# Optimization experiments

Measured on AMD Instinct MI355X. Metric: run time of the kernel, lower is better.

Reference implementation:

```python
import jax, jax.numpy as jnp
import numpy as np

ALPHA = 0.1        # dt / tau = 1 / 10
SIGMA_REC = 0.03
SIGMA_INP = 0.03


def setup_inputs() -> dict:
    key = jax.random.key(0)
    ks = jax.random.split(key, 7)
    n, N, num_inputs, num_outputs, T, B = 128, 1024, 6, 2, 512, 256
    u = jax.random.normal(ks[0], (num_inputs, T, B), dtype=jnp.float32)
    rec_noise = jax.random.normal(ks[1], (B, T, n), dtype=jnp.float32)
    inp_noise = jax.random.normal(ks[2], (B, T, num_inputs), dtype=jnp.float32)
    W_inp = jax.random.normal(ks[3], (n, num_inputs), dtype=jnp.float32) / np.float32(np.sqrt(num_inputs))
    # spectral-ish scaling keeps the leaky RNN stable over 512 steps
    W_rec = jax.random.normal(ks[4], (n, n), dtype=jnp.float32) * np.float32(0.9 / np.sqrt(n))
    W_out = jax.random.normal(ks[5], (num_outputs, n), dtype=jnp.float32) / np.float32(np.sqrt(n))
    # q is orthonormalized via SVD in the torch module (make_orthonormal)
    q0 = np.asarray(jax.random.uniform(ks[6], (n, N)), dtype=np.float32)
    U, _, Vh = np.linalg.svd(q0, full_matrices=False)
    q = jnp.asarray((U @ Vh).astype(np.float32))
    return dict(u=u, rec_noise=rec_noise, inp_noise=inp_noise,
                W_inp=W_inp, W_rec=W_rec, W_out=W_out, q=q)


def reference(u, rec_noise, inp_noise, W_inp, W_rec, W_out, q):
    # u: (num_inputs, T, B); noise tensors already batch-major (B, T, .)
    B = u.shape[-1]
    n = W_rec.shape[0]
    rn = jnp.sqrt(2.0 / ALPHA * SIGMA_REC ** 2) * rec_noise      # (B, T, n)
    inoise = jnp.sqrt(2.0 / ALPHA * SIGMA_INP ** 2) * inp_noise  # (B, T, num_inputs)
    ub = jnp.swapaxes(u, 0, -1)                                  # (B, T, num_inputs)
    x0 = jnp.zeros((B, n), dtype=u.dtype)                        # initial state self.x = 0

    def step(x, ins):
        u_t, in_t, rn_t = ins
        x_new = (1.0 - ALPHA) * x + ALPHA * (
            jax.nn.relu(x @ W_rec.T + (u_t + in_t) @ W_inp.T) + rn_t)
        return x_new, x_new

    # T-1 update steps using inputs at t = 0 .. T-2 (matches the torch loop)
    xs_in = (jnp.swapaxes(ub, 0, 1)[:-1],
             jnp.swapaxes(inoise, 0, 1)[:-1],
             jnp.swapaxes(rn, 0, 1)[:-1])
    _, xs = jax.lax.scan(step, x0, xs_in)                        # (T-1, B, n)
    states = jnp.concatenate([x0[:, None, :], jnp.swapaxes(xs, 0, 1)], axis=1)  # (B, T, n)

    outputs = jnp.swapaxes(states @ W_out.T, 0, -1)              # (num_outputs, T, B)
    states_embedded = jnp.swapaxes(states @ q, 0, -1)            # (N, T, B)
    return states_embedded, outputs
```

## Files before the change

### kernel.cpp

```cpp
#include <hip/hip_runtime.h>
#include <hip/hip_bf16.h>

#define T_STEPS 512
#define BATCH   256
#define NN      128
#define NEMB    1024
#define M_ROWS  (T_STEPS * BATCH)
#define NOISE_K 0.13416407864998738f
#define CH      8
#define NCHUNK  (T_STEPS / CH)

typedef short s16x8 __attribute__((ext_vector_type(8)));
typedef float f32x4 __attribute__((ext_vector_type(4)));

__device__ __forceinline__ unsigned short f2bf(float f) {
  union { float f; unsigned u; } v; v.f = f;
  unsigned r = v.u + 0x7fffu + ((v.u >> 16) & 1u);
  return (unsigned short)(r >> 16);
}
__device__ __forceinline__ float bf2f(unsigned short s) {
  union { unsigned u; float f; } v; v.u = ((unsigned)s) << 16;
  return v.f;
}
__device__ __forceinline__ float rdlane(float v, int l) {
  return __uint_as_float(__builtin_amdgcn_readlane(__float_as_uint(v), l));
}

__device__ __forceinline__ void light_barrier() {
  asm volatile("s_waitcnt lgkmcnt(0)" ::: "memory");
  __builtin_amdgcn_s_barrier();
  asm volatile("" ::: "memory");
}

__global__ __launch_bounds__(128, 1) void rnn_step_kernel(
    const float* __restrict__ u,
    const float* __restrict__ rec_noise,
    const float* __restrict__ inp_noise,
    const float* __restrict__ W_inp,
    const float* __restrict__ W_rec,
    unsigned short* __restrict__ states)
{
  const int b    = blockIdx.x;
  const int tid  = threadIdx.x;
  const int lane = tid & 63;

  __shared__ float xbuf[2][NN];
  __shared__ float rns[2][CH * NN];
  __shared__ float us[2][CH][8];

  const f32x4* wr = (const f32x4*)(W_rec + tid * NN);
  f32x4 w4[32];
  #pragma unroll
  for (int c = 0; c < 32; ++c) w4[c] = wr[c];

  float winp[6];
  #pragma unroll
  for (int j = 0; j < 6; ++j) winp[j] = W_inp[tid * 6 + j];

  const int ts6 = tid / 6, j6 = tid - ts6 * 6;

  xbuf[0][tid] = 0.f;
  states[b * NN + tid] = 0;

  {
    const f32x4* src = (const f32x4*)(rec_noise + (size_t)b * T_STEPS * NN);
    *(f32x4*)&rns[0][tid * 8]     = src[tid * 2];
    *(f32x4*)&rns[0][tid * 8 + 4] = src[tid * 2 + 1];
    if (tid < 48) {
      float uu = u[j6 * (T_STEPS * BATCH) + ts6 * BATCH + b];
      float in = inp_noise[((size_t)b * T_STEPS + ts6) * 6 + j6];
      us[0][ts6][j6] = uu + NOISE_K * in;
    }
  }
  __syncthreads();

  float xr = 0.f;
  for (int c = 0; c < NCHUNK; ++c) {
    const int cb = c & 1;

    f32x4 pf0 = {0.f, 0.f, 0.f, 0.f}, pf1 = {0.f, 0.f, 0.f, 0.f};
    float u_pf = 0.f, in_pf = 0.f;
    if (c < NCHUNK - 1) {
      const f32x4* src =
          (const f32x4*)(rec_noise + ((size_t)b * T_STEPS + (c + 1) * CH) * NN);
      pf0 = src[tid * 2];
      pf1 = src[tid * 2 + 1];
      if (tid < 48) {
        const int tt = (c + 1) * CH + ts6;
        u_pf  = u[j6 * (T_STEPS * BATCH) + tt * BATCH + b];
        in_pf = inp_noise[((size_t)b * T_STEPS + tt) * 6 + j6];
      }
    }

    #pragma unroll
    for (int ts = 0; ts < CH; ++ts) {
      const int t = c * CH + ts;
      if (t > T_STEPS - 2) break;
      const int cur = ts & 1, nxt = cur ^ 1;

      float2 vx = *(const float2*)&xbuf[cur][lane * 2];

      float a0 = 0.f, a1 = 0.f, a2 = 0.f, a3 = 0.f;
      #pragma unroll
      for (int kp = 0; kp < 64; ++kp) {
        const float x0 = rdlane(vx.x, kp);
        const float x1 = rdlane(vx.y, kp);
        const float we0 = w4[kp >> 1][(kp & 1) * 2];
        const float we1 = w4[kp >> 1][(kp & 1) * 2 + 1];
        if (kp & 1) { a2 = fmaf(we0, x0, a2); a3 = fmaf(we1, x1, a3); }
        else        { a0 = fmaf(we0, x0, a0); a1 = fmaf(we1, x1, a1); }
      }
      float acc = (a0 + a1) + (a2 + a3);

      float inp = 0.f;
      #pragma unroll
      for (int j = 0; j < 6; ++j) inp = fmaf(winp[j], us[cb][ts][j], inp);

      const float pre = acc + inp;
      const float r   = pre > 0.f ? pre : 0.f;
      const float xn  = 0.9f * xr + 0.1f * (r + NOISE_K * rns[cb][ts * NN + tid]);
      xr = xn;

      xbuf[nxt][tid] = xn;
      states[((t + 1) * BATCH + b) * NN + tid] = f2bf(xn);

      light_barrier();
    }

    if (c < NCHUNK - 1) {
      *(f32x4*)&rns[cb ^ 1][tid * 8]     = pf0;
      *(f32x4*)&rns[cb ^ 1][tid * 8 + 4] = pf1;
      if (tid < 48) us[cb ^ 1][ts6][j6] = u_pf + NOISE_K * in_pf;
      light_barrier();
    }
  }
}

__global__ __launch_bounds__(256) void emb_kernel(
    const unsigned short* __restrict__ states,
    const float* __restrict__ q,
    const float* __restrict__ W_out,
    float* __restrict__ out)
{
  const int jt  = blockIdx.x;
  const int mt  = blockIdx.y;
  const int tid = threadIdx.x;
  const int w   = tid >> 6;
  const int l   = tid & 63;
  const int lg  = l >> 4;
  const int lr  = l & 15;

  __shared__ unsigned short qt[64 * 128];
  __shared__ float wos[2 * NN];

  {
    const int j  = tid & 63;
    const int k0 = tid >> 6;
    #pragma unroll
    for (int kk = k0; kk < 128; kk += 4) {
      float v = q[kk * NEMB + jt * 64 + j];
      int k8 = kk >> 3, e = kk & 7;
      qt[j * 128 + ((k8 ^ (j & 7)) << 3) + e] = f2bf(v);
    }
  }
  if (jt == 0) wos[tid] = W_out[tid];

  s16x8 afrag[2][4];
  #pragma unroll
  for (int mf = 0; mf < 2; ++mf) {
    const int m = mt * 128 + w * 32 + mf * 16 + lr;
    const unsigned short* arow = states + m * NN;
    #pragma unroll
    for (int kc = 0; kc < 4; ++kc)
      afrag[mf][kc] = *(const s16x8*)(arow + kc * 32 + lg * 8);
  }
  __syncthreads();

  f32x4 acc[2][4] = {};
  #pragma unroll
  for (int kc = 0; kc < 4; ++kc) {
    s16x8 bfrag[4];
    #pragma unroll
    for (int jf = 0; jf < 4; ++jf) {
      const int jl = jf * 16 + lr;
      bfrag[jf] = *(const s16x8*)(qt + jl * 128 + ((((kc << 2) + lg) ^ (jl & 7)) << 3));
    }
    #pragma unroll
    for (int mf = 0; mf < 2; ++mf)
      #pragma unroll
      for (int jf = 0; jf < 4; ++jf)
        acc[mf][jf] = __builtin_amdgcn_mfma_f32_16x16x32_bf16(
            afrag[mf][kc], bfrag[jf], acc[mf][jf], 0, 0, 0);
  }

  if (jt == 0) {
    #pragma unroll
    for (int mf = 0; mf < 2; ++mf) {
      float s0 = 0.f, s1 = 0.f;
      #pragma unroll
      for (int kc = 0; kc < 4; ++kc) {
        const int kb = kc * 32 + lg * 8;
        const s16x8 af = afrag[mf][kc];
        #pragma unroll
        for (int e = 0; e < 8; ++e) {
          const float x = bf2f((unsigned short)af[e]);
          s0 = fmaf(x, wos[kb + e], s0);
          s1 = fmaf(x, wos[NN + kb + e], s1);
        }
      }
      s0 += __shfl_xor(s0, 16); s0 += __shfl_xor(s0, 32);
      s1 += __shfl_xor(s1, 16); s1 += __shfl_xor(s1, 32);
      if (lg == 0) {
        const long m = (long)mt * 128 + w * 32 + mf * 16 + lr;
        out[(long)1024 * M_ROWS + m] = s0;
        out[(long)1025 * M_ROWS + m] = s1;
      }
    }
  }

  #pragma unroll
  for (int mf = 0; mf < 2; ++mf) {
    const int m = mt * 128 + w * 32 + mf * 16 + lg * 4;
    #pragma unroll
    for (int jf = 0; jf < 4; ++jf) {
      const long j = jt * 64 + jf * 16 + lr;
      *(f32x4*)&out[j * M_ROWS + m] = acc[mf][jf];
    }
  }
}

extern "C" void kernel_launch(void* const* d_in, const int* in_sizes, int n_in,
                              void* d_out, int out_size, void* d_ws, size_t ws_size,
                              hipStream_t stream) {
  const float* u         = (const float*)d_in[0];
  const float* rec_noise = (const float*)d_in[1];
  const float* inp_noise = (const float*)d_in[2];
  const float* W_inp     = (const float*)d_in[3];
  const float* W_rec     = (const float*)d_in[4];
  const float* W_out     = (const float*)d_in[5];
  const float* q         = (const float*)d_in[6];
  float* out = (float*)d_out;
  unsigned short* states = (unsigned short*)d_ws;

  rnn_step_kernel<<<dim3(BATCH), dim3(128), 0, stream>>>(
      u, rec_noise, inp_noise, W_inp, W_rec, states);

  dim3 g2(NEMB / 64, M_ROWS / 128);
  emb_kernel<<<g2, dim3(256), 0, stream>>>(states, q, W_out, out);
}
```

Baseline: 467.7 us.

## Run RNN recurrence on MFMA with 16 batch rows per single-wave block

Replaces the per-batch 128-thread recurrence, which used readlane broadcasts and FMAs, with a single-wave kernel that handles 16 batch elements per block. Each step runs as bf16 MFMAs: W_rec and W_inp stay in registers as A fragments, and the state comes back through a small LDS tile in bf16. Rec-noise prefetch now uses async global_load_lds with an XOR swizzle, and block-wide barriers go away because each block is one wave. In exchange, the recurrent state and weights are rounded to bf16 every step, which may compound error over 511 steps, and only 16 workgroups run the serial phase.

```diff
diff --git a/kernel.cpp b/kernel.cpp
--- a/kernel.cpp
+++ b/kernel.cpp
@@ -7,11 +7,17 @@
 #define NEMB    1024
 #define M_ROWS  (T_STEPS * BATCH)
 #define NOISE_K 0.13416407864998738f
-#define CH      8
-#define NCHUNK  (T_STEPS / CH)
+#define NB      16
+#define CH      4
+#define NSTEP   (T_STEPS - 1)
+#define NCH     ((NSTEP + CH - 1) / CH)
 
 typedef short s16x8 __attribute__((ext_vector_type(8)));
 typedef float f32x4 __attribute__((ext_vector_type(4)));
+typedef int   s32x2 __attribute__((ext_vector_type(2)));
+typedef int   s32x4 __attribute__((ext_vector_type(4)));
+
+union FragU { s32x4 i4; s16x8 s8; };
 
 __device__ __forceinline__ unsigned short f2bf(float f) {
   union { float f; unsigned u; } v; v.f = f;
@@ -22,17 +28,12 @@
   union { unsigned u; float f; } v; v.u = ((unsigned)s) << 16;
   return v.f;
 }
-__device__ __forceinline__ float rdlane(float v, int l) {
-  return __uint_as_float(__builtin_amdgcn_readlane(__float_as_uint(v), l));
-}
-
-__device__ __forceinline__ void light_barrier() {
-  asm volatile("s_waitcnt lgkmcnt(0)" ::: "memory");
-  __builtin_amdgcn_s_barrier();
-  asm volatile("" ::: "memory");
-}
-
-__global__ __launch_bounds__(128, 1) void rnn_step_kernel(
+__device__ __forceinline__ unsigned pkbf(float lo, float hi) {
+  __hip_bfloat162 h = __float22bfloat162_rn(float2{lo, hi});
+  union { __hip_bfloat162 h; unsigned u; } c; c.h = h; return c.u;
+}
+
+__global__ __launch_bounds__(64, 1) void rnn_mfma_kernel(
     const float* __restrict__ u,
     const float* __restrict__ rec_noise,
     const float* __restrict__ inp_noise,
@@ -40,98 +41,160 @@
     const float* __restrict__ W_rec,
     unsigned short* __restrict__ states)
 {
-  const int b    = blockIdx.x;
-  const int tid  = threadIdx.x;
-  const int lane = tid & 63;
-
-  __shared__ float xbuf[2][NN];
-  __shared__ float rns[2][CH * NN];
-  __shared__ float us[2][CH][8];
-
-  const f32x4* wr = (const f32x4*)(W_rec + tid * NN);
-  f32x4 w4[32];
-  #pragma unroll
-  for (int c = 0; c < 32; ++c) w4[c] = wr[c];
-
-  float winp[6];
-  #pragma unroll
-  for (int j = 0; j < 6; ++j) winp[j] = W_inp[tid * 6 + j];
-
-  const int ts6 = tid / 6, j6 = tid - ts6 * 6;
-
-  xbuf[0][tid] = 0.f;
-  states[b * NN + tid] = 0;
-
+  const int b0 = blockIdx.x * NB;
+  const int l  = threadIdx.x;
+  const int lr = l & 15;
+  const int lg = l >> 4;
+
+  __shared__ char           xld[32 * 136];
+  __shared__ float          rns[2][NB * CH * 128];
+  __shared__ unsigned short uinl[NB * CH * 8];
+
+  s16x8 wA[8][5];
+  #pragma unroll
+  for (int mf = 0; mf < 8; ++mf) {
+    const float* wrow = W_rec + (size_t)(mf * 16 + lr) * NN;
+    #pragma unroll
+    for (int kc = 0; kc < 4; ++kc) {
+      f32x4 v0 = *(const f32x4*)(wrow + kc * 32 + lg * 8);
+      f32x4 v1 = *(const f32x4*)(wrow + kc * 32 + lg * 8 + 4);
+      FragU f;
+      f.i4 = s32x4{(int)pkbf(v0.x, v0.y), (int)pkbf(v0.z, v0.w),
+                   (int)pkbf(v1.x, v1.y), (int)pkbf(v1.z, v1.w)};
+      wA[mf][kc] = f.s8;
+    }
+    float wi[8] = {0.f, 0.f, 0.f, 0.f, 0.f, 0.f, 0.f, 0.f};
+    if (lg == 0) {
+      #pragma unroll
+      for (int j = 0; j < 6; ++j) wi[j] = W_inp[(mf * 16 + lr) * 6 + j];
+    }
+    FragU f;
+    f.i4 = s32x4{(int)pkbf(wi[0], wi[1]), (int)pkbf(wi[2], wi[3]),
+                 (int)pkbf(wi[4], wi[5]), (int)pkbf(wi[6], wi[7])};
+    wA[mf][4] = f.s8;
+  }
+
+  #pragma unroll
+  for (int i = 0; i < 17; ++i) ((int*)xld)[l + 64 * i] = 0;
+  #pragma unroll
+  for (int i = 0; i < 4; ++i)
+    *(s32x4*)((char*)states + (size_t)b0 * 256 + (l + 64 * i) * 16) =
+        s32x4{0, 0, 0, 0};
+
+  int loff[8];
+  #pragma unroll
+  for (int s = 0; s < 8; ++s)
+    loff[s] = (l >> 5) * 512 + (((l & 31) * 16) ^ (s << 4));
+
+  #pragma unroll
+  for (int b = 0; b < NB; ++b) {
+    const char* gb = (const char*)rec_noise +
+                     ((size_t)(b0 + b) * T_STEPS + 0) * 512 + loff[b & 7];
+    float* db = &rns[0][b * 512];
+    __builtin_amdgcn_global_load_lds(
+        (const __attribute__((address_space(1))) void*)gb,
+        (__attribute__((address_space(3))) void*)db, 16, 0, 0);
+    __builtin_amdgcn_global_load_lds(
+        (const __attribute__((address_space(1))) void*)(gb + 1024),
+        (__attribute__((address_space(3))) void*)(db + 256), 16, 0, 0);
+  }
+  float uu[6], ii[6];
   {
-    const f32x4* src = (const f32x4*)(rec_noise + (size_t)b * T_STEPS * NN);
-    *(f32x4*)&rns[0][tid * 8]     = src[tid * 2];
-    *(f32x4*)&rns[0][tid * 8 + 4] = src[tid * 2 + 1];
-    if (tid < 48) {
-      float uu = u[j6 * (T_STEPS * BATCH) + ts6 * BATCH + b];
-      float in = inp_noise[((size_t)b * T_STEPS + ts6) * 6 + j6];
-      us[0][ts6][j6] = uu + NOISE_K * in;
-    }
-  }
-  __syncthreads();
-
-  float xr = 0.f;
-  for (int c = 0; c < NCHUNK; ++c) {
+    const int tb = lg;
+    #pragma unroll
+    for (int j = 0; j < 6; ++j) {
+      uu[j] = u[(size_t)j * (T_STEPS * BATCH) + (size_t)tb * BATCH + b0 + lr];
+      ii[j] = inp_noise[((size_t)(b0 + lr) * T_STEPS + tb) * 6 + j];
+    }
+  }
+  asm volatile("s_waitcnt vmcnt(0)" ::: "memory");
+  {
+    s32x2 w01{(int)pkbf(uu[0] + NOISE_K * ii[0], uu[1] + NOISE_K * ii[1]),
+              (int)pkbf(uu[2] + NOISE_K * ii[2], uu[3] + NOISE_K * ii[3])};
+    s32x2 w23{(int)pkbf(uu[4] + NOISE_K * ii[4], uu[5] + NOISE_K * ii[5]), 0};
+    *(s32x2*)&uinl[(lr * 4 + lg) * 8]     = w01;
+    *(s32x2*)&uinl[(lr * 4 + lg) * 8 + 4] = w23;
+  }
+
+  float xo[8][4];
+  #pragma unroll
+  for (int mf = 0; mf < 8; ++mf)
+    #pragma unroll
+    for (int r = 0; r < 4; ++r) xo[mf][r] = 0.f;
+
+  for (int c = 0; c < NCH; ++c) {
     const int cb = c & 1;
-
-    f32x4 pf0 = {0.f, 0.f, 0.f, 0.f}, pf1 = {0.f, 0.f, 0.f, 0.f};
-    float u_pf = 0.f, in_pf = 0.f;
-    if (c < NCHUNK - 1) {
-      const f32x4* src =
-          (const f32x4*)(rec_noise + ((size_t)b * T_STEPS + (c + 1) * CH) * NN);
-      pf0 = src[tid * 2];
-      pf1 = src[tid * 2 + 1];
-      if (tid < 48) {
-        const int tt = (c + 1) * CH + ts6;
-        u_pf  = u[j6 * (T_STEPS * BATCH) + tt * BATCH + b];
-        in_pf = inp_noise[((size_t)b * T_STEPS + tt) * 6 + j6];
+    if (c > 0) {
+      asm volatile("s_waitcnt vmcnt(32)" ::: "memory");
+      s32x2 w01{(int)pkbf(uu[0] + NOISE_K * ii[0], uu[1] + NOISE_K * ii[1]),
+                (int)pkbf(uu[2] + NOISE_K * ii[2], uu[3] + NOISE_K * ii[3])};
+      s32x2 w23{(int)pkbf(uu[4] + NOISE_K * ii[4], uu[5] + NOISE_K * ii[5]), 0};
+      *(s32x2*)&uinl[(lr * 4 + lg) * 8]     = w01;
+      *(s32x2*)&uinl[(lr * 4 + lg) * 8 + 4] = w23;
+    }
+    if (c + 1 < NCH) {
+      const int t0 = (c + 1) * CH;
+      #pragma unroll
+      for (int b = 0; b < NB; ++b) {
+        const char* gb = (const char*)rec_noise +
+                         ((size_t)(b0 + b) * T_STEPS + t0) * 512 + loff[b & 7];
+        float* db = &rns[cb ^ 1][b * 512];
+        __builtin_amdgcn_global_load_lds(
+            (const __attribute__((address_space(1))) void*)gb,
+            (__attribute__((address_space(3))) void*)db, 16, 0, 0);
+        __builtin_amdgcn_global_load_lds(
+            (const __attribute__((address_space(1))) void*)(gb + 1024),
+            (__attribute__((address_space(3))) void*)(db + 256), 16, 0, 0);
+      }
+      const int tb = t0 + lg;
+      #pragma unroll
+      for (int j = 0; j < 6; ++j) {
+        uu[j] = u[(size_t)j * (T_STEPS * BATCH) + (size_t)tb * BATCH + b0 + lr];
+        ii[j] = inp_noise[((size_t)(b0 + lr) * T_STEPS + tb) * 6 + j];
       }
     }
 
     #pragma unroll
     for (int ts = 0; ts < CH; ++ts) {
       const int t = c * CH + ts;
-      if (t > T_STEPS - 2) break;
-      const int cur = ts & 1, nxt = cur ^ 1;
-
-      float2 vx = *(const float2*)&xbuf[cur][lane * 2];
-
-      float a0 = 0.f, a1 = 0.f, a2 = 0.f, a3 = 0.f;
-      #pragma unroll
-      for (int kp = 0; kp < 64; ++kp) {
-        const float x0 = rdlane(vx.x, kp);
-        const float x1 = rdlane(vx.y, kp);
-        const float we0 = w4[kp >> 1][(kp & 1) * 2];
-        const float we1 = w4[kp >> 1][(kp & 1) * 2 + 1];
-        if (kp & 1) { a2 = fmaf(we0, x0, a2); a3 = fmaf(we1, x1, a3); }
-        else        { a0 = fmaf(we0, x0, a0); a1 = fmaf(we1, x1, a1); }
-      }
-      float acc = (a0 + a1) + (a2 + a3);
-
-      float inp = 0.f;
-      #pragma unroll
-      for (int j = 0; j < 6; ++j) inp = fmaf(winp[j], us[cb][ts][j], inp);
-
-      const float pre = acc + inp;
-      const float r   = pre > 0.f ? pre : 0.f;
-      const float xn  = 0.9f * xr + 0.1f * (r + NOISE_K * rns[cb][ts * NN + tid]);
-      xr = xn;
-
-      xbuf[nxt][tid] = xn;
-      states[((t + 1) * BATCH + b) * NN + tid] = f2bf(xn);
-
-      light_barrier();
-    }
-
-    if (c < NCHUNK - 1) {
-      *(f32x4*)&rns[cb ^ 1][tid * 8]     = pf0;
-      *(f32x4*)&rns[cb ^ 1][tid * 8 + 4] = pf1;
-      if (tid < 48) us[cb ^ 1][ts6][j6] = u_pf + NOISE_K * in_pf;
-      light_barrier();
+      if (t >= NSTEP) break;
+
+      s16x8 xb[4];
+      #pragma unroll
+      for (int kc = 0; kc < 4; ++kc) {
+        const char* p = xld + (kc * 8 + lg * 2) * 136 + lr * 8;
+        s32x2 r1 = *(const s32x2*)p;
+        s32x2 r2 = *(const s32x2*)(p + 136);
+        FragU f; f.i4 = s32x4{r1.x, r1.y, r2.x, r2.y};
+        xb[kc] = f.s8;
+      }
+      FragU uf; uf.i4 = *(const s32x4*)&uinl[(lr * 4 + ts) * 8];
+      const s16x8 ub = (lg == 0) ? uf.s8 : s16x8{0, 0, 0, 0, 0, 0, 0, 0};
+
+      unsigned short* srow =
+          states + ((size_t)(t + 1) * BATCH + b0 + lr) * NN + lg * 4;
+
+      #pragma unroll
+      for (int mf = 0; mf < 8; ++mf) {
+        f32x4 a = f32x4{0.f, 0.f, 0.f, 0.f};
+        a = __builtin_amdgcn_mfma_f32_16x16x32_bf16(wA[mf][0], xb[0], a, 0, 0, 0);
+        a = __builtin_amdgcn_mfma_f32_16x16x32_bf16(wA[mf][1], xb[1], a, 0, 0, 0);
+        a = __builtin_amdgcn_mfma_f32_16x16x32_bf16(wA[mf][2], xb[2], a, 0, 0, 0);
+        a = __builtin_amdgcn_mfma_f32_16x16x32_bf16(wA[mf][3], xb[3], a, 0, 0, 0);
+        a = __builtin_amdgcn_mfma_f32_16x16x32_bf16(wA[mf][4], ub,    a, 0, 0, 0);
+        const f32x4 rn4 = *(const f32x4*)&rns[cb][lr * 512 + ts * 128 +
+                               ((mf * 16 + lg * 4) ^ ((lr & 7) << 2))];
+        float xn[4];
+        #pragma unroll
+        for (int r = 0; r < 4; ++r) {
+          const float rl = fmaxf(a[r], 0.f);
+          xn[r] = 0.9f * xo[mf][r] + 0.1f * (rl + NOISE_K * rn4[r]);
+          xo[mf][r] = xn[r];
+        }
+        const s32x2 pw{(int)pkbf(xn[0], xn[1]), (int)pkbf(xn[2], xn[3])};
+        *(s32x2*)(xld + (mf * 4 + lg) * 136 + lr * 8) = pw;
+        *(s32x2*)(srow + mf * 16) = pw;
+      }
     }
   }
 }
@@ -242,7 +305,7 @@
   float* out = (float*)d_out;
   unsigned short* states = (unsigned short*)d_ws;
 
-  rnn_step_kernel<<<dim3(BATCH), dim3(128), 0, stream>>>(
+  rnn_mfma_kernel<<<dim3(BATCH / NB), dim3(64), 0, stream>>>(
       u, rec_noise, inp_noise, W_inp, W_rec, states);
 
   dim3 g2(NEMB / 64, M_ROWS / 128);
```

New measurement: 777.6 us. +66.3%, slower.
